# Performance work log

Hardware: AMD Instinct MI355X
Metric: run time of the kernel (lower is better)

The kernel has to match this reference:

```python
import jax, jax.numpy as jnp
import numpy as np

D_MODEL = 2048
D_INNER = 2048          # expand=1
N_HEADS = 32            # n_qk_heads == n_v_heads
D_STATE = 64
HEADDIM = D_INNER // N_HEADS  # 64
D_CONV = 4
CHUNK = 128
D_FF = 8192
EPS = 1e-5
CONV_DIM = D_INNER + 2 * N_HEADS * D_STATE            # 6144
D_IN_PROJ = 2 * D_INNER + 2 * N_HEADS * D_STATE + N_HEADS  # 8224


def rmsnorm(x, w, eps=EPS):
    x32 = x.astype(jnp.float32)
    x32 = x32 * jax.lax.rsqrt(jnp.mean(x32 * x32, axis=-1, keepdims=True) + eps)
    return (w * x32).astype(x.dtype)


def causal_conv1d(x, w, b):
    # x: (B, L, C), w: (C, K) depthwise, b: (C,). Causal left padding (K-1).
    K = w.shape[1]
    y = jax.lax.conv_general_dilated(
        x, jnp.transpose(w)[:, None, :],  # (K, 1, C)
        window_strides=(1,), padding=[(K - 1, 0)],
        dimension_numbers=("NWC", "WIO", "NWC"),
        feature_group_count=x.shape[-1])
    return y + b


def ssd_scan(x, dt, Bm, Cm, chunk=CHUNK):
    # Discrete Mamba2 SSD: h_t = exp(-softplus(dt_t)) * h_{t-1} + B_t (x) x_t; y_t = C_t . h_t
    # x: (b,l,h,p), dt: (b,l,h), Bm/Cm: (b,l,h,n)
    b, l, h, p = x.shape
    n = Bm.shape[-1]
    c = l // chunk
    xr = x.reshape(b, c, chunk, h, p)
    a_log = (-jax.nn.softplus(dt)).reshape(b, c, chunk, h)  # per-step log decay
    Br = Bm.reshape(b, c, chunk, h, n)
    Cr = Cm.reshape(b, c, chunk, h, n)
    cum = jnp.cumsum(a_log, axis=2)  # inclusive cumulative log-decay within chunk (b,c,q,h)
    # intra-chunk: scores[i,j] = exp(cum_i - cum_j) * (C_i . B_j), causal j <= i
    seg = jnp.exp(cum[:, :, :, None, :] - cum[:, :, None, :, :])       # (b,c,i,j,h)
    cb = jnp.einsum("bcihn,bcjhn->bcijh", Cr, Br)
    mask = jnp.tril(jnp.ones((chunk, chunk), bool))
    scores = jnp.where(mask[None, None, :, :, None], seg * cb, 0.0)
    y_intra = jnp.einsum("bcijh,bcjhp->bcihp", scores, xr)
    # per-chunk end state contribution
    decay_to_end = jnp.exp(cum[:, :, -1:, :] - cum)                     # (b,c,q,h)
    S = jnp.einsum("bcqh,bcqhn,bcqhp->bchnp", decay_to_end, Br, xr)
    A_chunk = jnp.exp(cum[:, :, -1, :])                                  # (b,c,h)
    def step(hprev, inp):
        Ac, Sc = inp
        return Ac[..., None, None] * hprev + Sc, hprev
    h0 = jnp.zeros((b, h, n, p), x.dtype)
    _, Hprev = jax.lax.scan(step, h0, (jnp.moveaxis(A_chunk, 1, 0), jnp.moveaxis(S, 1, 0)))
    Hprev = jnp.moveaxis(Hprev, 0, 1)  # state at each chunk start (b,c,h,n,p)
    y_inter = jnp.einsum("bcqh,bcqhn,bchnp->bcqhp", jnp.exp(cum), Cr, Hprev)
    return (y_intra + y_inter).reshape(b, l, h, p)


def mixer(u, in_proj_w, z_bias, conv_w, conv_b, D, out_proj_w):
    b, l, _ = u.shape
    zxbcdt = u @ in_proj_w.T  # (b,l,8224)
    z = zxbcdt[..., :D_INNER]
    xBC = zxbcdt[..., D_INNER:D_INNER + CONV_DIM]
    dt = zxbcdt[..., D_INNER + CONV_DIM:]  # (b,l,H)
    xBC = causal_conv1d(xBC, conv_w, conv_b)  # activation = identity
    x = xBC[..., :D_INNER].reshape(b, l, N_HEADS, HEADDIM)
    Bm = xBC[..., D_INNER:D_INNER + N_HEADS * D_STATE].reshape(b, l, N_HEADS, D_STATE)
    Cm = xBC[..., D_INNER + N_HEADS * D_STATE:].reshape(b, l, N_HEADS, D_STATE)
    y = ssd_scan(x, dt, Bm, Cm)
    y = y + D[None, None, :, None] * x  # D skip
    y = y.reshape(b, l, D_INNER)
    return (y * jax.nn.silu(z + z_bias)) @ out_proj_w.T


def setup_inputs() -> dict:
    key = jax.random.key(0)
    ks = jax.random.split(key, 8)
    s = 0.02
    return {
        "hidden_states": jax.random.normal(ks[0], (2, 2048, D_MODEL), jnp.float32),
        "in_proj_w": jax.random.normal(ks[1], (D_IN_PROJ, D_MODEL), jnp.float32) * s,
        "z_bias": jnp.zeros((D_INNER,), jnp.float32),
        "conv_w": jax.random.normal(ks[2], (CONV_DIM, D_CONV), jnp.float32) * s,
        "conv_b": jnp.zeros((CONV_DIM,), jnp.float32),
        "D": jnp.ones((N_HEADS,), jnp.float32),
        "out_proj_w": jax.random.normal(ks[3], (D_MODEL, D_INNER), jnp.float32) * s,
        "norm1_w": jnp.ones((D_MODEL,), jnp.float32),
        "norm2_w": jnp.ones((D_MODEL,), jnp.float32),
        "gate_w": jax.random.normal(ks[4], (D_FF, D_MODEL), jnp.float32) * s,
        "up_w": jax.random.normal(ks[5], (D_FF, D_MODEL), jnp.float32) * s,
        "down_w": jax.random.normal(ks[6], (D_MODEL, D_FF), jnp.float32) * s,
    }


def reference(hidden_states, in_proj_w, z_bias, conv_w, conv_b, D, out_proj_w,
              norm1_w, norm2_w, gate_w, up_w, down_w):
    residual = hidden_states
    h = rmsnorm(hidden_states, norm1_w)
    h = mixer(h, in_proj_w, z_bias, conv_w, conv_b, D, out_proj_w) + residual
    residual = h
    h = rmsnorm(h, norm2_w)
    h = (jax.nn.silu(h @ gate_w.T) * (h @ up_w.T)) @ down_w.T  # LlamaMLP
    return residual + h
```

## Files before the change

kernel.cpp:

```cpp
#include <hip/hip_runtime.h>


typedef unsigned short u16;
typedef __bf16 bf16x8 __attribute__((ext_vector_type(8)));
typedef float f32x4 __attribute__((ext_vector_type(4)));

#define D_MODEL   2048
#define D_INNER   2048
#define NH        32
#define CONV_DIM  6144
#define D_IN_PROJ 8224
#define NPAD      8320
#define DFF       8192
#define BATCH     2
#define SEQ       2048
#define M_TOK     4096
#define NCHUNK    16
#define CHUNK     128

__device__ __forceinline__ u16 f2b(float f) {
  union { float f; unsigned int u; } v; v.f = f;
  unsigned int r = v.u + 0x7FFFu + ((v.u >> 16) & 1u);
  return (u16)(r >> 16);
}
__device__ __forceinline__ float b2f(u16 u) {
  union { unsigned int u; float f; } v; v.u = ((unsigned int)u) << 16; return v.f;
}

__device__ __forceinline__ void async16(const void* g, void* l) {
  __builtin_amdgcn_global_load_lds((const __attribute__((address_space(1))) void*)g,
                                   (__attribute__((address_space(3))) void*)l, 16, 0, 0);
}

template <int EPI>
__global__ void __launch_bounds__(256, 2) gemm_bt(
    const u16* __restrict__ A, const u16* __restrict__ W,
    float* Cf, u16* Cb, const float* auxf, const u16* auxb, float* Fdt,
    int K, int Nreal) {
  __shared__ __align__(16) u16 sA[128 * 32];
  __shared__ __align__(16) u16 sB[128 * 32];
  const int tid = threadIdx.x;
  const int bn = blockIdx.x, bm = blockIdx.y;
  const int lane = tid & 63;
  const int wave = tid >> 6;
  const int wm = (wave >> 1) * 64, wn = (wave & 1) * 64;

  const f32x4 zero4 = {0.f, 0.f, 0.f, 0.f};
  f32x4 acc[4][4];
#pragma unroll
  for (int i = 0; i < 4; ++i)
#pragma unroll
    for (int j = 0; j < 4; ++j) acc[i][j] = zero4;

  const int r0 = tid >> 2;
  const int kk = (tid & 3) * 8;
  const u16* ga0 = A + (size_t)(bm * 128 + r0) * K + kk;
  const u16* ga1 = ga0 + (size_t)64 * K;
  const u16* gb0 = W + (size_t)(bn * 128 + r0) * K + kk;
  const u16* gb1 = gb0 + (size_t)64 * K;
  u16* la0 = &sA[tid * 8]; u16* la1 = &sA[2048 + tid * 8];
  u16* lb0 = &sB[tid * 8]; u16* lb1 = &sB[2048 + tid * 8];

  const int lr = lane & 15;
  const int lk = (lane >> 4) * 8;

  for (int k0 = 0; k0 < K; k0 += 32) {
    async16(ga0, la0); async16(ga1, la1);
    async16(gb0, lb0); async16(gb1, lb1);
    ga0 += 32; ga1 += 32; gb0 += 32; gb1 += 32;
    __syncthreads();
    bf16x8 af[4], bfv[4];
#pragma unroll
    for (int mi = 0; mi < 4; ++mi)
      af[mi] = *(const bf16x8*)&sA[(wm + mi * 16 + lr) * 32 + lk];
#pragma unroll
    for (int ni = 0; ni < 4; ++ni)
      bfv[ni] = *(const bf16x8*)&sB[(wn + ni * 16 + lr) * 32 + lk];
#pragma unroll
    for (int mi = 0; mi < 4; ++mi)
#pragma unroll
      for (int ni = 0; ni < 4; ++ni)
        acc[mi][ni] = __builtin_amdgcn_mfma_f32_16x16x32_bf16(af[mi], bfv[ni], acc[mi][ni], 0, 0, 0);
    __syncthreads();
  }

  const int er = (lane >> 4) * 4;
  const int ec = lane & 15;
#pragma unroll
  for (int mi = 0; mi < 4; ++mi) {
#pragma unroll
    for (int r = 0; r < 4; ++r) {
      const int grow = bm * 128 + wm + mi * 16 + er + r;
#pragma unroll
      for (int ni = 0; ni < 4; ++ni) {
        const int gcol = bn * 128 + wn + ni * 16 + ec;
        if (gcol < Nreal) {
          const size_t idx = (size_t)grow * Nreal + gcol;
          const float v = acc[mi][ni][r];
          if (EPI == 1) {
            Cf[idx] = v + auxf[idx];
          } else if (EPI == 2) {
            const float g = b2f(auxb[idx]);
            const float sg = 1.f / (1.f + __expf(-g));
            Cb[idx] = f2b(v * g * sg);
          } else if (EPI == 3) {
            Cb[idx] = f2b(v);
            if (gcol >= D_INNER + CONV_DIM) Fdt[(size_t)grow * NH + (gcol - (D_INNER + CONV_DIM))] = v;
          } else {
            Cb[idx] = f2b(v);
          }
        }
      }
    }
  }
}

__global__ void cvt_kernel(const float* __restrict__ s, u16* __restrict__ d, int n4) {
  const int i = blockIdx.x * 256 + threadIdx.x;
  if (i >= n4) return;
  const float4 v = ((const float4*)s)[i];
  ushort4 r;
  r.x = f2b(v.x); r.y = f2b(v.y); r.z = f2b(v.z); r.w = f2b(v.w);
  ((ushort4*)d)[i] = r;
}

__global__ void rmsnorm_kernel(const float* __restrict__ x, const float* __restrict__ w,
                               u16* __restrict__ o) {
  const int row = blockIdx.x;
  const float* xr = x + (size_t)row * D_MODEL;
  float ss = 0.f;
  for (int c = threadIdx.x; c < D_MODEL; c += 256) { const float v = xr[c]; ss += v * v; }
#pragma unroll
  for (int off = 32; off > 0; off >>= 1) ss += __shfl_down(ss, off, 64);
  __shared__ float red[4];
  if ((threadIdx.x & 63) == 0) red[threadIdx.x >> 6] = ss;
  __syncthreads();
  const float scale = rsqrtf((red[0] + red[1] + red[2] + red[3]) * (1.f / D_MODEL) + 1e-5f);
  u16* orow = o + (size_t)row * D_MODEL;
  for (int c = threadIdx.x; c < D_MODEL; c += 256) orow[c] = f2b(xr[c] * scale * w[c]);
}

__global__ void conv_kernel(const u16* __restrict__ zx, const float* __restrict__ cw,
                            const float* __restrict__ cb, u16* __restrict__ out) {
  const int idx = blockIdx.x * 256 + threadIdx.x;
  const int ch = idx % CONV_DIM;
  const int m = idx / CONV_DIM;
  const int l = m & (SEQ - 1);
  float accv = cb[ch];
#pragma unroll
  for (int k = 0; k < 4; ++k) {
    const int ls = l - 3 + k;
    if (ls >= 0) accv += cw[ch * 4 + k] * b2f(zx[(size_t)(m - 3 + k) * D_IN_PROJ + D_INNER + ch]);
  }
  out[idx] = f2b(accv);
}

__global__ void dtcum_kernel(const float* __restrict__ dtbuf, float* __restrict__ cum) {
  const int blk = blockIdx.x;
  const int h = blk & 31, cc = (blk >> 5) & 15, b = blk >> 9;
  const int i = threadIdx.x;
  const int m = b * SEQ + cc * CHUNK + i;
  const float dt = dtbuf[(size_t)m * NH + h];
  const float sp = (dt > 20.f) ? dt : log1pf(__expf(dt));
  __shared__ float s[128];
  s[i] = -sp;
  __syncthreads();
  for (int off = 1; off < 128; off <<= 1) {
    const float v = (i >= off) ? s[i - off] : 0.f;
    __syncthreads();
    s[i] += v;
    __syncthreads();
  }
  cum[(size_t)m * NH + h] = s[i];
}

__global__ void state_kernel(const u16* __restrict__ xbc, const float* __restrict__ cum,
                             float* __restrict__ S) {
  const int blk = blockIdx.x;
  const int h = blk & 31, cc = (blk >> 5) & 15, b = blk >> 9;
  const int m0 = b * SEQ + cc * CHUNK;
  const int tid = threadIdx.x;
  const int tp = tid & 63, tg = tid >> 6;
  const int n0 = tg * 16;
  const float cl = cum[(size_t)(m0 + 127) * NH + h];
  __shared__ float sBq[32][64], sxq[32][64], sd[32];
  float accv[16];
#pragma unroll
  for (int i = 0; i < 16; ++i) accv[i] = 0.f;
  for (int q0 = 0; q0 < 128; q0 += 32) {
    __syncthreads();
    for (int e = tid; e < 2048; e += 256) {
      const int q = e >> 6, col = e & 63;
      const size_t rowb = (size_t)(m0 + q0 + q) * CONV_DIM;
      sBq[q][col] = b2f(xbc[rowb + D_INNER + h * 64 + col]);
      sxq[q][col] = b2f(xbc[rowb + h * 64 + col]);
    }
    if (tid < 32) sd[tid] = __expf(cl - cum[(size_t)(m0 + q0 + tid) * NH + h]);
    __syncthreads();
    for (int q = 0; q < 32; ++q) {
      const float xv = sxq[q][tp] * sd[q];
#pragma unroll
      for (int i = 0; i < 16; ++i) accv[i] += sBq[q][n0 + i] * xv;
    }
  }
  float* Sp = S + (((size_t)(b * 16 + cc) * NH + h) * 64) * 64;
#pragma unroll
  for (int i = 0; i < 16; ++i) Sp[(size_t)(n0 + i) * 64 + tp] = accv[i];
}

__global__ void scan_kernel(const float* __restrict__ S, const float* __restrict__ cum,
                            float* __restrict__ H) {
  const int idx = blockIdx.x * 256 + threadIdx.x;
  const int p = idx & 63, n = (idx >> 6) & 63, h = (idx >> 12) & 31, b = idx >> 17;
  float hs = 0.f;
  for (int cc = 0; cc < NCHUNK; ++cc) {
    const size_t off = (((size_t)(b * 16 + cc) * NH + h) * 64 + n) * 64 + p;
    H[off] = hs;
    const float Ac = __expf(cum[(size_t)(b * SEQ + cc * CHUNK + 127) * NH + h]);
    hs = Ac * hs + S[off];
  }
}

#define SPITCH 136
#define CPITCH 72
__global__ void __launch_bounds__(256, 2) y_kernel(
    const u16* __restrict__ xbc, const float* __restrict__ cum,
    const float* __restrict__ H, const float* __restrict__ Dp,
    const u16* __restrict__ zx, const float* __restrict__ zb,
    u16* __restrict__ yo) {
  const int blk = blockIdx.x;
  const int h = blk & 31, cc = (blk >> 5) & 15, b = blk >> 9;
  const int m0 = b * SEQ + cc * CHUNK;
  const int tid = threadIdx.x;
  const int lane = tid & 63, wave = tid >> 6;

  __shared__ __align__(16) u16 sC[128 * CPITCH];
  __shared__ __align__(16) u16 sU[64 * SPITCH + 64 * CPITCH];
  __shared__ __align__(16) u16 sP[128 * SPITCH];
  __shared__ float sCum[128];
  u16* sB = sU;
  u16* sxT = sU;
  u16* sHT = sU + 64 * SPITCH;

  {
    const int i = tid >> 4, n4 = (tid & 15) * 4;
    for (int i0 = 0; i0 < 128; i0 += 16) {
      const size_t g = (size_t)(m0 + i0 + i) * CONV_DIM + h * 64 + n4;
      *(ushort4*)&sC[(i0 + i) * CPITCH + n4] = *(const ushort4*)&xbc[g + 2 * D_INNER];
      *(ushort4*)&sB[(i0 + i) * CPITCH + n4] = *(const ushort4*)&xbc[g + D_INNER];
    }
    if (tid < 128) sCum[tid] = cum[(size_t)(m0 + tid) * NH + h];
  }
  __syncthreads();

  const int lr = lane & 15;
  const int lk = (lane >> 4) * 8;
  const int er = (lane >> 4) * 4;
  const int ec = lane & 15;

  {
    const int R = (wave >> 1) * 64, Cq = (wave & 1) * 64;
    const f32x4 z4 = {0.f, 0.f, 0.f, 0.f};
    f32x4 acc[4][4];
#pragma unroll
    for (int i = 0; i < 4; ++i)
#pragma unroll
      for (int j = 0; j < 4; ++j) acc[i][j] = z4;
#pragma unroll
    for (int k0 = 0; k0 < 64; k0 += 32) {
      bf16x8 af[4], bfv[4];
#pragma unroll
      for (int mi = 0; mi < 4; ++mi)
        af[mi] = *(const bf16x8*)&sC[(R + mi * 16 + lr) * CPITCH + k0 + lk];
#pragma unroll
      for (int ni = 0; ni < 4; ++ni)
        bfv[ni] = *(const bf16x8*)&sB[(Cq + ni * 16 + lr) * CPITCH + k0 + lk];
#pragma unroll
      for (int mi = 0; mi < 4; ++mi)
#pragma unroll
        for (int ni = 0; ni < 4; ++ni)
          acc[mi][ni] = __builtin_amdgcn_mfma_f32_16x16x32_bf16(af[mi], bfv[ni], acc[mi][ni], 0, 0, 0);
    }
#pragma unroll
    for (int mi = 0; mi < 4; ++mi)
#pragma unroll
      for (int r = 0; r < 4; ++r) {
        const int row = R + mi * 16 + er + r;
#pragma unroll
        for (int ni = 0; ni < 4; ++ni) {
          const int col = Cq + ni * 16 + ec;
          const float pv = (row >= col) ? __expf(sCum[row] - sCum[col]) * acc[mi][ni][r] : 0.f;
          sP[row * SPITCH + col] = f2b(pv);
        }
      }
  }
  __syncthreads();

  {
    const int i = tid >> 1, n32 = (tid & 1) * 32;
    const float sc = __expf(sCum[i]);
    for (int n = n32; n < n32 + 32; ++n)
      sC[i * CPITCH + n] = f2b(b2f(sC[i * CPITCH + n]) * sc);
  }
  {
    const int j = tid >> 1, p32 = (tid & 1) * 32;
    const size_t g = (size_t)(m0 + j) * CONV_DIM + h * 64;
    for (int p = p32; p < p32 + 32; ++p)
      sxT[p * SPITCH + j] = xbc[g + p];
    const float* Hp = H + (((size_t)(b * 16 + cc) * NH + h) * 64) * 64;
    if (j < 64) {
      const int n = j;
      for (int p = p32; p < p32 + 32; ++p)
        sHT[p * CPITCH + n] = f2b(Hp[n * 64 + p]);
    }
  }
  __syncthreads();

  {
    const int R2 = wave * 32;
    const f32x4 z4 = {0.f, 0.f, 0.f, 0.f};
    f32x4 acc[2][4];
#pragma unroll
    for (int i = 0; i < 2; ++i)
#pragma unroll
      for (int j = 0; j < 4; ++j) acc[i][j] = z4;
#pragma unroll
    for (int k0 = 0; k0 < 128; k0 += 32) {
      bf16x8 af[2], bfv[4];
#pragma unroll
      for (int mi = 0; mi < 2; ++mi)
        af[mi] = *(const bf16x8*)&sP[(R2 + mi * 16 + lr) * SPITCH + k0 + lk];
#pragma unroll
      for (int ni = 0; ni < 4; ++ni)
        bfv[ni] = *(const bf16x8*)&sxT[(ni * 16 + lr) * SPITCH + k0 + lk];
#pragma unroll
      for (int mi = 0; mi < 2; ++mi)
#pragma unroll
        for (int ni = 0; ni < 4; ++ni)
          acc[mi][ni] = __builtin_amdgcn_mfma_f32_16x16x32_bf16(af[mi], bfv[ni], acc[mi][ni], 0, 0, 0);
    }
#pragma unroll
    for (int k0 = 0; k0 < 64; k0 += 32) {
      bf16x8 af[2], bfv[4];
#pragma unroll
      for (int mi = 0; mi < 2; ++mi)
        af[mi] = *(const bf16x8*)&sC[(R2 + mi * 16 + lr) * CPITCH + k0 + lk];
#pragma unroll
      for (int ni = 0; ni < 4; ++ni)
        bfv[ni] = *(const bf16x8*)&sHT[(ni * 16 + lr) * CPITCH + k0 + lk];
#pragma unroll
      for (int mi = 0; mi < 2; ++mi)
#pragma unroll
        for (int ni = 0; ni < 4; ++ni)
          acc[mi][ni] = __builtin_amdgcn_mfma_f32_16x16x32_bf16(af[mi], bfv[ni], acc[mi][ni], 0, 0, 0);
    }
    const float Dh = Dp[h];
#pragma unroll
    for (int mi = 0; mi < 2; ++mi)
#pragma unroll
      for (int r = 0; r < 4; ++r) {
        const int row = R2 + mi * 16 + er + r;
        const int m = m0 + row;
#pragma unroll
        for (int ni = 0; ni < 4; ++ni) {
          const int p = ni * 16 + ec;
          const int gc = h * 64 + p;
          const float xv = b2f(sxT[p * SPITCH + row]);
          const float z = b2f(zx[(size_t)m * D_IN_PROJ + gc]) + zb[gc];
          const float sg = 1.f / (1.f + __expf(-z));
          yo[(size_t)m * D_INNER + gc] = f2b((acc[mi][ni][r] + Dh * xv) * z * sg);
        }
      }
  }
}

extern "C" void kernel_launch(void* const* d_in, const int* in_sizes, int n_in,
                              void* d_out, int out_size, void* d_ws, size_t ws_size,
                              hipStream_t stream) {
  (void)in_sizes; (void)n_in; (void)out_size; (void)ws_size;
  const float* hidden = (const float*)d_in[0];
  const float* w_in   = (const float*)d_in[1];
  const float* z_bias = (const float*)d_in[2];
  const float* conv_w = (const float*)d_in[3];
  const float* conv_b = (const float*)d_in[4];
  const float* Dp     = (const float*)d_in[5];
  const float* w_out  = (const float*)d_in[6];
  const float* n1w    = (const float*)d_in[7];
  const float* n2w    = (const float*)d_in[8];
  const float* w_g    = (const float*)d_in[9];
  const float* w_u    = (const float*)d_in[10];
  const float* w_d    = (const float*)d_in[11];
  float* out = (float*)d_out;

  char* p = (char*)d_ws;
  auto take = [&](size_t bytes) { char* r = p; p += (bytes + 255) & ~(size_t)255; return r; };
  u16*   Bzx  = (u16*)take((size_t)M_TOK * D_IN_PROJ * 2);
  u16*   Bxbc = (u16*)take((size_t)M_TOK * CONV_DIM * 2);
  float* F_cum = (float*)take((size_t)M_TOK * NH * 4);
  float* F_S   = (float*)take((size_t)BATCH * NCHUNK * NH * 64 * 64 * 4);
  float* F_H   = (float*)take((size_t)BATCH * NCHUNK * NH * 64 * 64 * 4);
  u16*   B_h   = (u16*)take((size_t)M_TOK * D_MODEL * 2);
  float* F_dt  = (float*)take((size_t)M_TOK * NH * 4);
  u16*   W_buf = (u16*)take((size_t)NPAD * D_MODEL * 2);
  u16* B_y    = (u16*)F_S;
  u16* B_gate = Bzx;
  u16* B_gu   = Bxbc;
  float* F_res2 = out;

  const int c2 = (D_MODEL * D_INNER / 4 + 255) / 256;
  const int c8 = (DFF * D_MODEL / 4 + 255) / 256;

  cvt_kernel<<<(D_IN_PROJ * D_MODEL / 4 + 255) / 256, 256, 0, stream>>>(w_in, W_buf, D_IN_PROJ * D_MODEL / 4);
  rmsnorm_kernel<<<M_TOK, 256, 0, stream>>>(hidden, n1w, B_h);
  gemm_bt<3><<<dim3(NPAD / 128, M_TOK / 128), 256, 0, stream>>>(B_h, W_buf, nullptr, Bzx, nullptr, nullptr, F_dt, D_MODEL, D_IN_PROJ);

  conv_kernel<<<M_TOK * CONV_DIM / 256, 256, 0, stream>>>(Bzx, conv_w, conv_b, Bxbc);
  dtcum_kernel<<<BATCH * NCHUNK * NH, 128, 0, stream>>>(F_dt, F_cum);
  state_kernel<<<BATCH * NCHUNK * NH, 256, 0, stream>>>(Bxbc, F_cum, F_S);
  scan_kernel<<<BATCH * NH * 64 * 64 / 256, 256, 0, stream>>>(F_S, F_cum, F_H);
  y_kernel<<<BATCH * NCHUNK * NH, 256, 0, stream>>>(Bxbc, F_cum, F_H, Dp, Bzx, z_bias, B_y);

  cvt_kernel<<<c2, 256, 0, stream>>>(w_out, W_buf, D_MODEL * D_INNER / 4);
  gemm_bt<1><<<dim3(D_MODEL / 128, M_TOK / 128), 256, 0, stream>>>(B_y, W_buf, F_res2, nullptr, hidden, nullptr, nullptr, D_INNER, D_MODEL);

  rmsnorm_kernel<<<M_TOK, 256, 0, stream>>>(F_res2, n2w, B_h);
  cvt_kernel<<<c8, 256, 0, stream>>>(w_g, W_buf, DFF * D_MODEL / 4);
  gemm_bt<4><<<dim3(DFF / 128, M_TOK / 128), 256, 0, stream>>>(B_h, W_buf, nullptr, B_gate, nullptr, nullptr, nullptr, D_MODEL, DFF);
  cvt_kernel<<<c8, 256, 0, stream>>>(w_u, W_buf, DFF * D_MODEL / 4);
  gemm_bt<2><<<dim3(DFF / 128, M_TOK / 128), 256, 0, stream>>>(B_h, W_buf, nullptr, B_gu, nullptr, B_gate, nullptr, D_MODEL, DFF);
  cvt_kernel<<<c8, 256, 0, stream>>>(w_d, W_buf, D_MODEL * DFF / 4);
  gemm_bt<1><<<dim3(D_MODEL / 128, M_TOK / 128), 256, 0, stream>>>(B_gu, W_buf, out, nullptr, F_res2, nullptr, nullptr, DFF, D_MODEL);
}
```

Measured before the change: 1.350 ms.

## Add grouped block swizzle and 128x64 tiles for narrow-N GEMMs

Switches the GEMM grid to a 1D launch with an 8-row grouped swizzle so that neighbouring blocks share A and W tiles in L2. Adds a TN=64 tile variant, used for the two N=2048 output projections (out_proj and down_proj), which doubles their block count for better CU fill. Raises the launch-bounds occupancy hint from 2 to 4 blocks per CU, which may force register spilling in the 128x128 variant. The smaller tiles also give less reuse per block.

New measurement: 1.346 ms. Within noise of the previous version (-0.3%).

```diff
diff --git a/kernel.cpp b/kernel.cpp
--- a/kernel.cpp
+++ b/kernel.cpp
@@ -32,23 +32,29 @@
                                    (__attribute__((address_space(3))) void*)l, 16, 0, 0);
 }
 
-template <int EPI>
-__global__ void __launch_bounds__(256, 2) gemm_bt(
+template <int EPI, int TN>
+__global__ void __launch_bounds__(256, 4) gemm_bt(
     const u16* __restrict__ A, const u16* __restrict__ W,
     float* Cf, u16* Cb, const float* auxf, const u16* auxb, float* Fdt,
     int K, int Nreal) {
+  constexpr int MI = (TN == 128) ? 4 : 2;
   __shared__ __align__(16) u16 sA[128 * 32];
-  __shared__ __align__(16) u16 sB[128 * 32];
+  __shared__ __align__(16) u16 sB[TN * 32];
   const int tid = threadIdx.x;
-  const int bn = blockIdx.x, bm = blockIdx.y;
+  const int grid_n = gridDim.x >> 5;
+  const int span = grid_n << 3;
+  const int pid = blockIdx.x;
+  const int bm = ((pid / span) << 3) + ((pid % span) & 7);
+  const int bn = (pid % span) >> 3;
   const int lane = tid & 63;
   const int wave = tid >> 6;
-  const int wm = (wave >> 1) * 64, wn = (wave & 1) * 64;
+  const int wm = (TN == 128) ? (wave >> 1) * 64 : wave * 32;
+  const int wn = (TN == 128) ? (wave & 1) * 64 : 0;
 
   const f32x4 zero4 = {0.f, 0.f, 0.f, 0.f};
-  f32x4 acc[4][4];
-#pragma unroll
-  for (int i = 0; i < 4; ++i)
+  f32x4 acc[MI][4];
+#pragma unroll
+  for (int i = 0; i < MI; ++i)
 #pragma unroll
     for (int j = 0; j < 4; ++j) acc[i][j] = zero4;
 
@@ -56,28 +62,30 @@
   const int kk = (tid & 3) * 8;
   const u16* ga0 = A + (size_t)(bm * 128 + r0) * K + kk;
   const u16* ga1 = ga0 + (size_t)64 * K;
-  const u16* gb0 = W + (size_t)(bn * 128 + r0) * K + kk;
+  const u16* gb0 = W + (size_t)(bn * TN + r0) * K + kk;
   const u16* gb1 = gb0 + (size_t)64 * K;
   u16* la0 = &sA[tid * 8]; u16* la1 = &sA[2048 + tid * 8];
-  u16* lb0 = &sB[tid * 8]; u16* lb1 = &sB[2048 + tid * 8];
+  u16* lb0 = &sB[tid * 8]; u16* lb1 = (TN == 128) ? &sB[2048 + tid * 8] : nullptr;
 
   const int lr = lane & 15;
   const int lk = (lane >> 4) * 8;
 
   for (int k0 = 0; k0 < K; k0 += 32) {
     async16(ga0, la0); async16(ga1, la1);
-    async16(gb0, lb0); async16(gb1, lb1);
-    ga0 += 32; ga1 += 32; gb0 += 32; gb1 += 32;
-    __syncthreads();
-    bf16x8 af[4], bfv[4];
-#pragma unroll
-    for (int mi = 0; mi < 4; ++mi)
+    async16(gb0, lb0);
+    if (TN == 128) async16(gb1, lb1);
+    ga0 += 32; ga1 += 32; gb0 += 32;
+    if (TN == 128) gb1 += 32;
+    __syncthreads();
+    bf16x8 af[MI], bfv[4];
+#pragma unroll
+    for (int mi = 0; mi < MI; ++mi)
       af[mi] = *(const bf16x8*)&sA[(wm + mi * 16 + lr) * 32 + lk];
 #pragma unroll
     for (int ni = 0; ni < 4; ++ni)
       bfv[ni] = *(const bf16x8*)&sB[(wn + ni * 16 + lr) * 32 + lk];
 #pragma unroll
-    for (int mi = 0; mi < 4; ++mi)
+    for (int mi = 0; mi < MI; ++mi)
 #pragma unroll
       for (int ni = 0; ni < 4; ++ni)
         acc[mi][ni] = __builtin_amdgcn_mfma_f32_16x16x32_bf16(af[mi], bfv[ni], acc[mi][ni], 0, 0, 0);
@@ -87,13 +95,13 @@
   const int er = (lane >> 4) * 4;
   const int ec = lane & 15;
 #pragma unroll
-  for (int mi = 0; mi < 4; ++mi) {
+  for (int mi = 0; mi < MI; ++mi) {
 #pragma unroll
     for (int r = 0; r < 4; ++r) {
       const int grow = bm * 128 + wm + mi * 16 + er + r;
 #pragma unroll
       for (int ni = 0; ni < 4; ++ni) {
-        const int gcol = bn * 128 + wn + ni * 16 + ec;
+        const int gcol = bn * TN + wn + ni * 16 + ec;
         if (gcol < Nreal) {
           const size_t idx = (size_t)grow * Nreal + gcol;
           const float v = acc[mi][ni][r];
@@ -412,7 +420,7 @@
 
   cvt_kernel<<<(D_IN_PROJ * D_MODEL / 4 + 255) / 256, 256, 0, stream>>>(w_in, W_buf, D_IN_PROJ * D_MODEL / 4);
   rmsnorm_kernel<<<M_TOK, 256, 0, stream>>>(hidden, n1w, B_h);
-  gemm_bt<3><<<dim3(NPAD / 128, M_TOK / 128), 256, 0, stream>>>(B_h, W_buf, nullptr, Bzx, nullptr, nullptr, F_dt, D_MODEL, D_IN_PROJ);
+  gemm_bt<3, 128><<<(NPAD / 128) * 32, 256, 0, stream>>>(B_h, W_buf, nullptr, Bzx, nullptr, nullptr, F_dt, D_MODEL, D_IN_PROJ);
 
   conv_kernel<<<M_TOK * CONV_DIM / 256, 256, 0, stream>>>(Bzx, conv_w, conv_b, Bxbc);
   dtcum_kernel<<<BATCH * NCHUNK * NH, 128, 0, stream>>>(F_dt, F_cum);
@@ -421,13 +429,13 @@
   y_kernel<<<BATCH * NCHUNK * NH, 256, 0, stream>>>(Bxbc, F_cum, F_H, Dp, Bzx, z_bias, B_y);
 
   cvt_kernel<<<c2, 256, 0, stream>>>(w_out, W_buf, D_MODEL * D_INNER / 4);
-  gemm_bt<1><<<dim3(D_MODEL / 128, M_TOK / 128), 256, 0, stream>>>(B_y, W_buf, F_res2, nullptr, hidden, nullptr, nullptr, D_INNER, D_MODEL);
+  gemm_bt<1, 64><<<(D_MODEL / 64) * 32, 256, 0, stream>>>(B_y, W_buf, F_res2, nullptr, hidden, nullptr, nullptr, D_INNER, D_MODEL);
 
   rmsnorm_kernel<<<M_TOK, 256, 0, stream>>>(F_res2, n2w, B_h);
   cvt_kernel<<<c8, 256, 0, stream>>>(w_g, W_buf, DFF * D_MODEL / 4);
-  gemm_bt<4><<<dim3(DFF / 128, M_TOK / 128), 256, 0, stream>>>(B_h, W_buf, nullptr, B_gate, nullptr, nullptr, nullptr, D_MODEL, DFF);
+  gemm_bt<4, 128><<<(DFF / 128) * 32, 256, 0, stream>>>(B_h, W_buf, nullptr, B_gate, nullptr, nullptr, nullptr, D_MODEL, DFF);
   cvt_kernel<<<c8, 256, 0, stream>>>(w_u, W_buf, DFF * D_MODEL / 4);
-  gemm_bt<2><<<dim3(DFF / 128, M_TOK / 128), 256, 0, stream>>>(B_h, W_buf, nullptr, B_gu, nullptr, B_gate, nullptr, D_MODEL, DFF);
+  gemm_bt<2, 128><<<(DFF / 128) * 32, 256, 0, stream>>>(B_h, W_buf, nullptr, B_gu, nullptr, B_gate, nullptr, D_MODEL, DFF);
   cvt_kernel<<<c8, 256, 0, stream>>>(w_d, W_buf, D_MODEL * DFF / 4);
-  gemm_bt<1><<<dim3(D_MODEL / 128, M_TOK / 128), 256, 0, stream>>>(B_gu, W_buf, out, nullptr, F_res2, nullptr, nullptr, DFF, D_MODEL);
-}
+  gemm_bt<1, 64><<<(D_MODEL / 64) * 32, 256, 0, stream>>>(B_gu, W_buf, out, nullptr, F_res2, nullptr, nullptr, DFF, D_MODEL);
+}
```
